# Kernel tuning notes

Hardware: AMD Instinct MI355X
Metric: run time of the kernel (lower is better)

The kernel has to match this reference:

```python
import jax, jax.numpy as jnp
import numpy as np
import math

H, W = 32, 32
HID = 256
K = 4
B = 16
DIN = 272
DFF = 1024
L = 2
NB = 7
IMG_H, IMG_W = 256, 256
LN_EPS = 1e-5


def _layernorm(x, g, b):
    m = jnp.mean(x, axis=-1, keepdims=True)
    v = jnp.var(x, axis=-1, keepdims=True)
    return (x - m) / jnp.sqrt(v + LN_EPS) * g + b


def _neighbor_mask(h, w, nb):
    # (h*w, h*w): 0 inside the nb x nb window around each query pixel, -inf outside
    rr = jnp.repeat(jnp.arange(h), w)
    cc = jnp.tile(jnp.arange(w), h)
    near = (jnp.abs(rr[:, None] - rr[None, :]) <= nb // 2) & (
        jnp.abs(cc[:, None] - cc[None, :]) <= nb // 2
    )
    return jnp.where(near, 0.0, -jnp.inf).astype(jnp.float32)


def _pos_embed(row_embed, col_embed):
    # pos[i*w + j] = concat(col_embed[j], row_embed[i])  -> (h*w, hid)
    h, nf = row_embed.shape
    w = col_embed.shape[0]
    pe = jnp.concatenate(
        [
            jnp.broadcast_to(col_embed[None, :, :], (h, w, nf)),
            jnp.broadcast_to(row_embed[:, None, :], (h, w, nf)),
        ],
        axis=-1,
    )
    return pe.reshape(h * w, 2 * nf)


def _resize_bilinear_ac(x, oh, ow):
    # nn.UpsamplingBilinear2d => align_corners=True
    b, c, h, w = x.shape
    ys = jnp.arange(oh) * ((h - 1) / (oh - 1))
    y0 = jnp.floor(ys).astype(jnp.int32)
    y1 = jnp.minimum(y0 + 1, h - 1)
    fy = (ys - y0).astype(x.dtype)
    x = x[:, :, y0, :] * (1 - fy)[None, None, :, None] + x[:, :, y1, :] * fy[None, None, :, None]
    xs = jnp.arange(ow) * ((w - 1) / (ow - 1))
    x0 = jnp.floor(xs).astype(jnp.int32)
    x1 = jnp.minimum(x0 + 1, w - 1)
    fx = (xs - x0).astype(x.dtype)
    x = x[:, :, :, x0] * (1 - fx) + x[:, :, :, x1] * fx
    return x


def _forward(query_features, matched_features, qW, qb, kvW, kvb, row_embed, col_embed,
             aggW, aggb, n1g, n1b, l1W, l1b, l2W, l2b, n2g, n2b, outW, outb):
    b, c_in, h, w = query_features.shape
    n = h * w
    # b c h w -> b (h w) c, then input projections
    qt = query_features.transpose(0, 2, 3, 1).reshape(b, n, c_in) @ qW + qb  # (b,n,hid)
    kt = matched_features.transpose(0, 1, 3, 4, 2).reshape(K, b, n, c_in) @ kvW + kvb  # (K,b,n,hid)

    pos = _pos_embed(row_embed, col_embed)  # (n, hid); broadcast over batch
    mask = _neighbor_mask(h, w, NB)  # (n, n)
    scale = 1.0 / math.sqrt(qt.shape[-1])

    x = qt
    for l in range(L):
        qp = (x + pos) * scale            # q gets pos embed then scaled
        kp = kt + pos                     # k gets pos embed; v is the raw matched tokens
        scores = jnp.einsum('bnc,kbmc->kbnm', qp, kp) + mask
        attn = jax.nn.softmax(scores, axis=-1)
        o = jnp.einsum('kbnm,kbmc->bnkc', attn, kt).reshape(b, n, K * HID)
        o = o @ aggW[l] + aggb[l]
        x = _layernorm(x + o, n1g[l], n1b[l])
        ff = jax.nn.relu(x @ l1W[l] + l1b[l]) @ l2W[l] + l2b[l]
        x = _layernorm(x + ff, n2g[l], n2b[l])

    recon_tokens = x @ outW + outb  # (b,n,c_in)
    recon = recon_tokens.reshape(b, h, w, c_in).transpose(0, 3, 1, 2)
    pred = jnp.sqrt(jnp.sum((recon - query_features) ** 2, axis=1, keepdims=True))
    pred = (pred - pred.min()) / (pred.max() - pred.min())
    pred = _resize_bilinear_ac(pred, IMG_H, IMG_W)
    return recon, pred


def setup_inputs() -> dict:
    key = jax.random.key(0)
    ks = jax.random.split(key, 12)

    def nrm(k, shape, scale=0.02):
        return jax.random.normal(k, shape, jnp.float32) * scale

    return {
        'query_features': jax.random.normal(ks[0], (B, DIN, H, W), jnp.float32),
        'matched_features': jax.random.normal(ks[1], (K, B, DIN, H, W), jnp.float32),
        'qW': nrm(ks[2], (DIN, HID)), 'qb': jnp.zeros((HID,), jnp.float32),
        'kvW': nrm(ks[3], (DIN, HID)), 'kvb': jnp.zeros((HID,), jnp.float32),
        'row_embed': jax.random.uniform(ks[4], (H, HID // 2), jnp.float32),
        'col_embed': jax.random.uniform(ks[5], (W, HID // 2), jnp.float32),
        'aggW': nrm(ks[6], (L, K * HID, HID)), 'aggb': jnp.zeros((L, HID), jnp.float32),
        'n1g': jnp.ones((L, HID), jnp.float32), 'n1b': jnp.zeros((L, HID), jnp.float32),
        'l1W': nrm(ks[7], (L, HID, DFF)), 'l1b': jnp.zeros((L, DFF), jnp.float32),
        'l2W': nrm(ks[8], (L, DFF, HID)), 'l2b': jnp.zeros((L, HID), jnp.float32),
        'n2g': jnp.ones((L, HID), jnp.float32), 'n2b': jnp.zeros((L, HID), jnp.float32),
        'outW': nrm(ks[9], (HID, DIN)), 'outb': jnp.zeros((DIN,), jnp.float32),
    }


def reference(query_features, matched_features, qW, qb, kvW, kvb, row_embed, col_embed,
              aggW, aggb, n1g, n1b, l1W, l1b, l2W, l2b, n2g, n2b, outW, outb):
    return _forward(query_features, matched_features, qW, qb, kvW, kvb, row_embed,
                    col_embed, aggW, aggb, n1g, n1b, l1W, l1b, l2W, l2b, n2g, n2b,
                    outW, outb)
```

## Files before the change

kernel.cpp:

```cpp
#include <hip/hip_runtime.h>
#include <hip/hip_bf16.h>
#include <math.h>

#define BATCH 16
#define NTOK 1024
#define HID 256
#define KMEM 4
#define DIN 272
#define DINP 288
#define DFF 1024
#define LN_EPS 1e-5f

using short8 = __attribute__((ext_vector_type(8))) short;
using short4v = __attribute__((ext_vector_type(4))) short;
using floatx4 = __attribute__((ext_vector_type(4))) float;

__device__ inline short f2bf(float f) {
  unsigned u = __builtin_bit_cast(unsigned, f);
  u += 0x7fff + ((u >> 16) & 1);
  return (short)(u >> 16);
}
__device__ inline float bf2f(short s) {
  unsigned u = ((unsigned)(unsigned short)s) << 16;
  return __builtin_bit_cast(float, u);
}

#define QSCALE 0.0625f

__global__ __launch_bounds__(256) void pos_kernel(
    const float* __restrict__ row_e, const float* __restrict__ col_e,
    float* __restrict__ pos) {
  int t = blockIdx.x;
  int j = threadIdx.x;
  float v = (j < 128) ? col_e[(t & 31) * 128 + j]
                      : row_e[(t >> 5) * 128 + (j - 128)];
  pos[t * 256 + j] = v;
}

struct WtJob {
  const float* src;
  short* dst;
  int K, Kd, N, ntx, start;
};
struct WtJobs {
  WtJob j[9];
};

__global__ __launch_bounds__(256) void wt_cvt_all_kernel(WtJobs jobs) {
  __shared__ short tile[32][33];
  int bid = blockIdx.x;
  int ji = 0;
#pragma unroll
  for (int i = 1; i < 9; ++i)
    if (bid >= jobs.j[i].start) ji = i;
  const float* W = jobs.j[ji].src;
  short* Wt = jobs.j[ji].dst;
  int K = jobs.j[ji].K, Kd = jobs.j[ji].Kd, N = jobs.j[ji].N;
  int local = bid - jobs.j[ji].start;
  int n0 = (local % jobs.j[ji].ntx) * 32;
  int k0 = (local / jobs.j[ji].ntx) * 32;
  int tx = threadIdx.x & 31, ty8 = threadIdx.x >> 5;
#pragma unroll
  for (int i = 0; i < 4; i++) {
    int k = k0 + ty8 + i * 8;
    int n = n0 + tx;
    float v = (k < K && n < N) ? W[(long)k * N + n] : 0.f;
    tile[ty8 + i * 8][tx] = f2bf(v);
  }
  __syncthreads();
#pragma unroll
  for (int i = 0; i < 4; i++) {
    int n = n0 + ty8 + i * 8;
    int k = k0 + tx;
    if (n < N && k < Kd) Wt[(long)n * Kd + k] = tile[tx][ty8 + i * 8];
  }
}

template <int OUTMODE, bool AFP32>
__global__ __launch_bounds__(256) void gemm2_kernel(
    const void* __restrict__ Ap, const short* __restrict__ Wt,
    const float* __restrict__ bias, float* __restrict__ Cf,
    short* __restrict__ Cs, int M, int N, int K, int gxn,
    short* __restrict__ ktp, short* __restrict__ ktv,
    const float* __restrict__ pos, const float* __restrict__ qfp,
    float* __restrict__ ppart) {
  __shared__ short As[2][64][40];
  __shared__ short Bs[2][128][40];
  __shared__ float part_s[64][2];
  int nwg = gridDim.x;
  int cpx = nwg >> 3;
  int bid = blockIdx.x;
  int h = (bid & 7) * cpx + (bid >> 3);
  int cx = h % gxn;
  int ry = h / gxn;
  int row0 = ry * 64, col0 = cx * 128;
  int tid = threadIdx.x;
  int w = tid >> 6, lane = tid & 63;
  int wrow = (w >> 1) * 32, wcol = (w & 1) * 64;
  int lcol = lane & 15, kg = lane >> 4;

  const short* Ab16 = nullptr;
  const float* Abf = nullptr;
  int arow = tid >> 2, ak = (tid & 3) * 8;
  int atok = tid & 63, acb = (tid >> 6) * 8;
  if (AFP32) {
    int slice = row0 >> 10, tok0 = row0 & 1023;
    Abf = (const float*)Ap + (long)slice * DIN * NTOK + tok0;
  } else {
    Ab16 = (const short*)Ap + (long)row0 * K;
  }
  int brow = tid >> 2, bk = (tid & 3) * 8;
  const short* Bb = Wt + (long)col0 * K;
  bool bv0 = (col0 + brow) < N;
  bool bv1 = (col0 + brow + 64) < N;

  const short8 z8 = (short8){0, 0, 0, 0, 0, 0, 0, 0};
  short8 ra;
  float rf[8];
  short8 rb0, rb1;
  if (AFP32) {
#pragma unroll
    for (int j = 0; j < 8; ++j)
      rf[j] = (acb + j < DIN) ? Abf[(long)(acb + j) * NTOK + atok] : 0.f;
    short8 s;
#pragma unroll
    for (int j = 0; j < 8; ++j) s[j] = f2bf(rf[j]);
    *reinterpret_cast<short8*>(&As[0][atok][acb]) = s;
  } else {
    ra = *reinterpret_cast<const short8*>(&Ab16[(long)arow * K + ak]);
    *reinterpret_cast<short8*>(&As[0][arow][ak]) = ra;
  }
  rb0 = bv0 ? *reinterpret_cast<const short8*>(&Bb[(long)brow * K + bk]) : z8;
  rb1 = bv1 ? *reinterpret_cast<const short8*>(&Bb[(long)(brow + 64) * K + bk])
            : z8;
  *reinterpret_cast<short8*>(&Bs[0][brow][bk]) = rb0;
  *reinterpret_cast<short8*>(&Bs[0][brow + 64][bk]) = rb1;
  __syncthreads();

  floatx4 acc[2][4];
#pragma unroll
  for (int m = 0; m < 2; ++m)
#pragma unroll
    for (int n = 0; n < 4; ++n) acc[m][n] = (floatx4){0.f, 0.f, 0.f, 0.f};

  int NT = K >> 5;
  for (int t = 0; t < NT; ++t) {
    int cur = t & 1;
    if (t + 1 < NT) {
      int ko = (t + 1) << 5;
      if (AFP32) {
#pragma unroll
        for (int j = 0; j < 8; ++j)
          rf[j] = (ko + acb + j < DIN)
                      ? Abf[(long)(ko + acb + j) * NTOK + atok]
                      : 0.f;
      } else {
        ra = *reinterpret_cast<const short8*>(&Ab16[(long)arow * K + ko + ak]);
      }
      rb0 = bv0 ? *reinterpret_cast<const short8*>(&Bb[(long)brow * K + ko + bk])
                : z8;
      rb1 = bv1 ? *reinterpret_cast<const short8*>(
                      &Bb[(long)(brow + 64) * K + ko + bk])
                : z8;
    }
    short8 af[2], bf[4];
#pragma unroll
    for (int m = 0; m < 2; ++m)
      af[m] = *reinterpret_cast<const short8*>(
          &As[cur][wrow + m * 16 + lcol][kg * 8]);
#pragma unroll
    for (int n = 0; n < 4; ++n)
      bf[n] = *reinterpret_cast<const short8*>(
          &Bs[cur][wcol + n * 16 + lcol][kg * 8]);
#pragma unroll
    for (int m = 0; m < 2; ++m)
#pragma unroll
      for (int n = 0; n < 4; ++n)
        acc[m][n] = __builtin_amdgcn_mfma_f32_16x16x32_bf16(af[m], bf[n],
                                                            acc[m][n], 0, 0, 0);
    if (t + 1 < NT) {
      int nxt = cur ^ 1;
      if (AFP32) {
        short8 s;
#pragma unroll
        for (int j = 0; j < 8; ++j) s[j] = f2bf(rf[j]);
        *reinterpret_cast<short8*>(&As[nxt][atok][acb]) = s;
      } else {
        *reinterpret_cast<short8*>(&As[nxt][arow][ak]) = ra;
      }
      *reinterpret_cast<short8*>(&Bs[nxt][brow][bk]) = rb0;
      *reinterpret_cast<short8*>(&Bs[nxt][brow + 64][bk]) = rb1;
    }
    __syncthreads();
  }

  if (OUTMODE == 2) {
    short* Ts = &Bs[0][0][0];
    int slice = row0 >> 10, tok0 = row0 & 1023;
#pragma unroll
    for (int n = 0; n < 4; ++n) {
      int cl = wcol + n * 16 + lcol;
      int c = col0 + cl;
      float bv = bias[c];
#pragma unroll
      for (int m = 0; m < 2; ++m) {
        int rl = wrow + m * 16 + kg * 4;
#pragma unroll
        for (int q = 0; q < 4; ++q) {
          float val = acc[m][n][q] + bv;
          Ts[(rl + q) * 132 + cl] = f2bf(val);
          ktp[(long)(row0 + rl + q) * 256 + c] =
              f2bf(val + pos[(tok0 + rl + q) * 256 + c]);
        }
      }
    }
    __syncthreads();
    int t8 = tid & 7;
#pragma unroll
    for (int p = 0; p < 4; ++p) {
      int cl = p * 32 + (tid >> 3);
      short8 v;
#pragma unroll
      for (int j = 0; j < 8; ++j) v[j] = Ts[(t8 * 8 + j) * 132 + cl];
      *reinterpret_cast<short8*>(
          &ktv[(long)slice * (256 * 1024) + (long)(col0 + cl) * 1024 + tok0 +
               t8 * 8]) = v;
    }
    return;
  }

  if (OUTMODE == 4) {
    int bb = row0 >> 10;
    int tb0 = (row0 & 1023) + wrow;
    float sqp[2][4] = {};
#pragma unroll
    for (int n = 0; n < 4; ++n) {
      int c = col0 + wcol + n * 16 + lcol;
      if (c < N) {
        float bv = bias[c];
#pragma unroll
        for (int m = 0; m < 2; ++m) {
          int tb = tb0 + m * 16 + kg * 4;
          long addr = ((long)bb * DIN + c) * 1024 + tb;
          float4 qv = *reinterpret_cast<const float4*>(&qfp[addr]);
          float4 ov;
          float v0 = acc[m][n][0] + bv;
          float v1 = acc[m][n][1] + bv;
          float v2 = acc[m][n][2] + bv;
          float v3 = acc[m][n][3] + bv;
          ov.x = v0;
          ov.y = v1;
          ov.z = v2;
          ov.w = v3;
          float d0 = v0 - qv.x, d1 = v1 - qv.y, d2 = v2 - qv.z, d3 = v3 - qv.w;
          sqp[m][0] = fmaf(d0, d0, sqp[m][0]);
          sqp[m][1] = fmaf(d1, d1, sqp[m][1]);
          sqp[m][2] = fmaf(d2, d2, sqp[m][2]);
          sqp[m][3] = fmaf(d3, d3, sqp[m][3]);
          *reinterpret_cast<float4*>(&Cf[addr]) = ov;
        }
      }
    }
#pragma unroll
    for (int m = 0; m < 2; ++m)
#pragma unroll
      for (int q = 0; q < 4; ++q) {
        float s = sqp[m][q];
        s += __shfl_xor(s, 1);
        s += __shfl_xor(s, 2);
        s += __shfl_xor(s, 4);
        s += __shfl_xor(s, 8);
        if (lcol == 0) part_s[wrow + m * 16 + kg * 4 + q][w & 1] = s;
      }
    __syncthreads();
    if (tid < 64)
      ppart[(long)cx * 16384 + row0 + tid] = part_s[tid][0] + part_s[tid][1];
    return;
  }

#pragma unroll
  for (int n = 0; n < 4; ++n) {
    int c = col0 + wcol + n * 16 + lcol;
    if (c >= N) continue;
    float bv = bias[c];
#pragma unroll
    for (int m = 0; m < 2; ++m) {
      int rbase = row0 + wrow + m * 16 + kg * 4;
      if (OUTMODE == 0) {
#pragma unroll
        for (int q = 0; q < 4; ++q)
          Cf[(long)(rbase + q) * N + c] = acc[m][n][q] + bv;
      } else if (OUTMODE == 1) {
#pragma unroll
        for (int q = 0; q < 4; ++q)
          Cs[(long)(rbase + q) * N + c] = f2bf(fmaxf(acc[m][n][q] + bv, 0.f));
      } else if (OUTMODE == 3) {
#pragma unroll
        for (int q = 0; q < 4; ++q) {
          float val = acc[m][n][q] + bv;
          Cf[(long)(rbase + q) * N + c] = val;
          Cs[(long)(rbase + q) * N + c] =
              f2bf((val + pos[((rbase + q) & 1023) * 256 + c]) * QSCALE);
        }
      }
    }
  }
}

template <bool EX, bool EQ>
__global__ __launch_bounds__(256) void gemm_ln_kernel(
    const short* __restrict__ A, const short* __restrict__ Wt,
    const float* __restrict__ bias, const float* __restrict__ res,
    const float* __restrict__ g, const float* __restrict__ bta,
    float* __restrict__ xout, short* __restrict__ x16out,
    const float* __restrict__ pos, short* __restrict__ q16out, int K) {
  __shared__ short As[2][32][40];
  __shared__ short Bs[2][256][40];
  __shared__ float st_s[32][4];
  __shared__ float st_s2[32][4];
  int tid = threadIdx.x;
  int row0 = blockIdx.x * 32;
  int w = tid >> 6, lane = tid & 63, lcol = lane & 15, kg = lane >> 4;
  int arow = tid >> 2, ak = (tid & 3) * 8;
  int brow = tid >> 2, bk = (tid & 3) * 8;
  const short* Ab = A + (long)row0 * K;

  short8 ra, rb[4];
  if (tid < 128) ra = *reinterpret_cast<const short8*>(&Ab[(long)arow * K + ak]);
#pragma unroll
  for (int i = 0; i < 4; ++i)
    rb[i] = *reinterpret_cast<const short8*>(&Wt[(long)(brow + i * 64) * K + bk]);
  if (tid < 128) *reinterpret_cast<short8*>(&As[0][arow][ak]) = ra;
#pragma unroll
  for (int i = 0; i < 4; ++i)
    *reinterpret_cast<short8*>(&Bs[0][brow + i * 64][bk]) = rb[i];
  __syncthreads();

  floatx4 acc[2][4];
#pragma unroll
  for (int m = 0; m < 2; ++m)
#pragma unroll
    for (int n = 0; n < 4; ++n) acc[m][n] = (floatx4){0.f, 0.f, 0.f, 0.f};

  int NT = K >> 5;
  for (int t = 0; t < NT; ++t) {
    int cur = t & 1;
    if (t + 1 < NT) {
      int ko = (t + 1) << 5;
      if (tid < 128)
        ra = *reinterpret_cast<const short8*>(&Ab[(long)arow * K + ko + ak]);
#pragma unroll
      for (int i = 0; i < 4; ++i)
        rb[i] = *reinterpret_cast<const short8*>(
            &Wt[(long)(brow + i * 64) * K + ko + bk]);
    }
    short8 af[2], bf[4];
#pragma unroll
    for (int m = 0; m < 2; ++m)
      af[m] =
          *reinterpret_cast<const short8*>(&As[cur][m * 16 + lcol][kg * 8]);
#pragma unroll
    for (int n = 0; n < 4; ++n)
      bf[n] = *reinterpret_cast<const short8*>(
          &Bs[cur][w * 64 + n * 16 + lcol][kg * 8]);
#pragma unroll
    for (int m = 0; m < 2; ++m)
#pragma unroll
      for (int n = 0; n < 4; ++n)
        acc[m][n] = __builtin_amdgcn_mfma_f32_16x16x32_bf16(af[m], bf[n],
                                                            acc[m][n], 0, 0, 0);
    if (t + 1 < NT) {
      int nxt = cur ^ 1;
      if (tid < 128) *reinterpret_cast<short8*>(&As[nxt][arow][ak]) = ra;
#pragma unroll
      for (int i = 0; i < 4; ++i)
        *reinterpret_cast<short8*>(&Bs[nxt][brow + i * 64][bk]) = rb[i];
    }
    __syncthreads();
  }

  float val[2][4][4];
#pragma unroll
  for (int n = 0; n < 4; ++n) {
    int c = w * 64 + n * 16 + lcol;
    float bv = bias[c];
#pragma unroll
    for (int m = 0; m < 2; ++m) {
      int rbase = row0 + m * 16 + kg * 4;
#pragma unroll
      for (int q = 0; q < 4; ++q)
        val[m][n][q] = acc[m][n][q] + bv + res[(long)(rbase + q) * 256 + c];
    }
  }
  float s[2][4], s2[2][4];
#pragma unroll
  for (int m = 0; m < 2; ++m)
#pragma unroll
    for (int q = 0; q < 4; ++q) {
      float ss = 0.f, ss2 = 0.f;
#pragma unroll
      for (int n = 0; n < 4; ++n) {
        float v = val[m][n][q];
        ss += v;
        ss2 = fmaf(v, v, ss2);
      }
      ss += __shfl_xor(ss, 1);
      ss2 += __shfl_xor(ss2, 1);
      ss += __shfl_xor(ss, 2);
      ss2 += __shfl_xor(ss2, 2);
      ss += __shfl_xor(ss, 4);
      ss2 += __shfl_xor(ss2, 4);
      ss += __shfl_xor(ss, 8);
      ss2 += __shfl_xor(ss2, 8);
      s[m][q] = ss;
      s2[m][q] = ss2;
    }
  if (lcol == 0) {
#pragma unroll
    for (int m = 0; m < 2; ++m)
#pragma unroll
      for (int q = 0; q < 4; ++q) {
        st_s[m * 16 + kg * 4 + q][w] = s[m][q];
        st_s2[m * 16 + kg * 4 + q][w] = s2[m][q];
      }
  }
  __syncthreads();
#pragma unroll
  for (int m = 0; m < 2; ++m)
#pragma unroll
    for (int q = 0; q < 4; ++q) {
      int row = m * 16 + kg * 4 + q;
      float4 a4 = *reinterpret_cast<const float4*>(&st_s[row][0]);
      float4 b4 = *reinterpret_cast<const float4*>(&st_s2[row][0]);
      float S = (a4.x + a4.y) + (a4.z + a4.w);
      float S2 = (b4.x + b4.y) + (b4.z + b4.w);
      float mean = S * (1.f / 256.f);
      float var = S2 * (1.f / 256.f) - mean * mean;
      float inv = rsqrtf(var + LN_EPS);
#pragma unroll
      for (int n = 0; n < 4; ++n) {
        int c = w * 64 + n * 16 + lcol;
        float o = (val[m][n][q] - mean) * inv * g[c] + bta[c];
        long addr = (long)(row0 + row) * 256 + c;
        if (EX) xout[addr] = o;
        x16out[addr] = f2bf(o);
        if (EQ)
          q16out[addr] =
              f2bf((o + pos[((row0 + row) & 1023) * 256 + c]) * QSCALE);
      }
    }
}

__global__ __launch_bounds__(256) void attn_kernel(
    const short* __restrict__ q16, const short* __restrict__ ktp,
    const short* __restrict__ ktv, short* __restrict__ o) {
  __shared__ short QP_s[32][264];
  __shared__ float st_mx[32][4];
  __shared__ float st_sm[32][4];
  int h = blockIdx.x;
  int xcd = h & 7, jj = h >> 3;
  int sidx = xcd * 8 + (jj >> 5);
  int r = jj & 31;
  int b = sidx & 15, k = sidx >> 4;
  int tid = threadIdx.x;
  int w = tid >> 6, lane = tid & 63, lcol = lane & 15, kg = lane >> 4;

  int r0 = max(r - 3, 0), r1 = min(r + 3, 31);
  int nkr = r1 - r0 + 1, nm = nkr * 32;
  const short* qb = q16 + ((long)b * NTOK + r * 32) * HID;
  const short* ktpb = ktp + ((long)(k * BATCH + b)) * NTOK * HID;
  const short* ktvb = ktv + ((long)(k * BATCH + b)) * NTOK * HID;

#pragma unroll
  for (int p = 0; p < 4; ++p) {
    int chunk = p * 256 + tid;
    int row = chunk >> 5, c8 = (chunk & 31) * 8;
    short8 v = *reinterpret_cast<const short8*>(&qb[(long)row * HID + c8]);
    *reinterpret_cast<short8*>(&QP_s[row][c8]) = v;
  }
  __syncthreads();

  floatx4 acc[2][4];
#pragma unroll
  for (int m = 0; m < 2; ++m)
#pragma unroll
    for (int n = 0; n < 4; ++n) acc[m][n] = (floatx4){0.f, 0.f, 0.f, 0.f};

  int tokn[4];
#pragma unroll
  for (int n = 0; n < 4; ++n) {
    int nf = w * 4 + n;
    int krow = min(r0 + (nf >> 1), 31);
    tokn[n] = krow * 32 + ((nf & 1) << 4) + lcol;
  }
#pragma unroll
  for (int s = 0; s < 8; ++s) {
    short8 af0 = *reinterpret_cast<const short8*>(&QP_s[lcol][s * 32 + kg * 8]);
    short8 af1 =
        *reinterpret_cast<const short8*>(&QP_s[16 + lcol][s * 32 + kg * 8]);
#pragma unroll
    for (int n = 0; n < 4; ++n) {
      short8 bfr = *reinterpret_cast<const short8*>(
          &ktpb[(long)tokn[n] * HID + s * 32 + kg * 8]);
      acc[0][n] =
          __builtin_amdgcn_mfma_f32_16x16x32_bf16(af0, bfr, acc[0][n], 0, 0, 0);
      acc[1][n] =
          __builtin_amdgcn_mfma_f32_16x16x32_bf16(af1, bfr, acc[1][n], 0, 0, 0);
    }
  }

  const float NEG = -3.0e38f;
  float mx[2][4];
#pragma unroll
  for (int m = 0; m < 2; ++m)
#pragma unroll
    for (int q = 0; q < 4; ++q) {
      int rr = m * 16 + kg * 4 + q;
      float vmax = NEG;
#pragma unroll
      for (int n = 0; n < 4; ++n) {
        int col = (w * 4 + n) * 16 + lcol;
        int ck = col & 31;
        bool ok = (col < nm) && (ck - rr <= 3) && (rr - ck <= 3);
        float v = ok ? acc[m][n][q] : NEG;
        acc[m][n][q] = v;
        vmax = fmaxf(vmax, v);
      }
      vmax = fmaxf(vmax, __shfl_xor(vmax, 1));
      vmax = fmaxf(vmax, __shfl_xor(vmax, 2));
      vmax = fmaxf(vmax, __shfl_xor(vmax, 4));
      vmax = fmaxf(vmax, __shfl_xor(vmax, 8));
      mx[m][q] = vmax;
    }
  if (lcol == 0) {
#pragma unroll
    for (int m = 0; m < 2; ++m)
#pragma unroll
      for (int q = 0; q < 4; ++q) st_mx[m * 16 + kg * 4 + q][w] = mx[m][q];
  }
  __syncthreads();
  float sm[2][4];
#pragma unroll
  for (int m = 0; m < 2; ++m)
#pragma unroll
    for (int q = 0; q < 4; ++q) {
      int rr = m * 16 + kg * 4 + q;
      float4 v4 = *reinterpret_cast<const float4*>(&st_mx[rr][0]);
      float g = fmaxf(fmaxf(v4.x, v4.y), fmaxf(v4.z, v4.w));
      float ss = 0.f;
#pragma unroll
      for (int n = 0; n < 4; ++n) {
        float v = acc[m][n][q];
        float pv = (v > -1.0e30f) ? exp2f((v - g) * 1.4426950408889634f) : 0.f;
        acc[m][n][q] = pv;
        ss += pv;
      }
      ss += __shfl_xor(ss, 1);
      ss += __shfl_xor(ss, 2);
      ss += __shfl_xor(ss, 4);
      ss += __shfl_xor(ss, 8);
      sm[m][q] = ss;
    }
  if (lcol == 0) {
#pragma unroll
    for (int m = 0; m < 2; ++m)
#pragma unroll
      for (int q = 0; q < 4; ++q) st_sm[m * 16 + kg * 4 + q][w] = sm[m][q];
  }
  __syncthreads();
#pragma unroll
  for (int m = 0; m < 2; ++m)
#pragma unroll
    for (int q = 0; q < 4; ++q) {
      int rr = m * 16 + kg * 4 + q;
      float4 v4 = *reinterpret_cast<const float4*>(&st_sm[rr][0]);
      float rinv = 1.0f / (v4.x + v4.y + v4.z + v4.w);
#pragma unroll
      for (int n = 0; n < 4; ++n) {
        QP_s[rr][(w * 4 + n) * 16 + lcol] = f2bf(acc[m][n][q] * rinv);
      }
    }
  __syncthreads();

  floatx4 oacc[2][4];
#pragma unroll
  for (int m = 0; m < 2; ++m)
#pragma unroll
    for (int n = 0; n < 4; ++n) oacc[m][n] = (floatx4){0.f, 0.f, 0.f, 0.f};

  for (int kb = 0; kb < nkr; ++kb) {
    short8 ap0 = *reinterpret_cast<const short8*>(&QP_s[lcol][kb * 32 + kg * 8]);
    short8 ap1 =
        *reinterpret_cast<const short8*>(&QP_s[16 + lcol][kb * 32 + kg * 8]);
    int tokb = (r0 + kb) * 32;
#pragma unroll
    for (int n = 0; n < 4; ++n) {
      int ch = w * 64 + n * 16 + lcol;
      short8 bv = *reinterpret_cast<const short8*>(
          &ktvb[(long)ch * NTOK + tokb + kg * 8]);
      oacc[0][n] =
          __builtin_amdgcn_mfma_f32_16x16x32_bf16(ap0, bv, oacc[0][n], 0, 0, 0);
      oacc[1][n] =
          __builtin_amdgcn_mfma_f32_16x16x32_bf16(ap1, bv, oacc[1][n], 0, 0, 0);
    }
  }
#pragma unroll
  for (int m = 0; m < 2; ++m)
#pragma unroll
    for (int n = 0; n < 4; ++n) {
      int ch = w * 64 + n * 16 + lcol;
#pragma unroll
      for (int q = 0; q < 4; ++q) {
        int rr = m * 16 + kg * 4 + q;
        o[((long)b * NTOK + r * 32 + rr) * (KMEM * HID) + k * HID + ch] =
            f2bf(oacc[m][n][q]);
      }
    }
}

__global__ __launch_bounds__(256) void minmax_kernel(
    const float* __restrict__ ppart, float* __restrict__ pred_sq,
    float* __restrict__ mnmx) {
  int tid = threadIdx.x;
  float mn = INFINITY, mx = -INFINITY;
  for (int i = tid; i < BATCH * NTOK; i += 256) {
    float v = ppart[i] + ppart[16384 + i] + ppart[32768 + i];
    pred_sq[i] = v;
    float sv = sqrtf(v);
    mn = fminf(mn, sv);
    mx = fmaxf(mx, sv);
  }
#pragma unroll
  for (int off = 32; off > 0; off >>= 1) {
    mn = fminf(mn, __shfl_xor(mn, off));
    mx = fmaxf(mx, __shfl_xor(mx, off));
  }
  __shared__ float smn[4], smx[4];
  int wave = tid >> 6, lane = tid & 63;
  if (lane == 0) {
    smn[wave] = mn;
    smx[wave] = mx;
  }
  __syncthreads();
  if (tid == 0) {
    mn = fminf(fminf(smn[0], smn[1]), fminf(smn[2], smn[3]));
    mx = fmaxf(fmaxf(smx[0], smx[1]), fmaxf(smx[2], smx[3]));
    mnmx[0] = mn;
    mnmx[1] = mx;
  }
}

__global__ __launch_bounds__(256) void resize_kernel(
    const float* __restrict__ pred_sq, const float* __restrict__ mnmx,
    float* __restrict__ out) {
  long idx = (long)blockIdx.x * 256 + threadIdx.x;
  if (idx >= (long)BATCH * 256 * 256) return;
  int b = (int)(idx >> 16);
  int oy = (int)((idx >> 8) & 255), ox = (int)(idx & 255);
  float mn = mnmx[0], mx = mnmx[1];
  float inv = 1.0f / (mx - mn);
  float ys = oy * (31.0f / 255.0f);
  int y0 = (int)floorf(ys);
  int y1 = min(y0 + 1, 31);
  float fy = ys - (float)y0;
  float xs = ox * (31.0f / 255.0f);
  int x0 = (int)floorf(xs);
  int x1 = min(x0 + 1, 31);
  float fx = xs - (float)x0;
  const float* p = pred_sq + b * NTOK;
  float v00 = sqrtf(p[y0 * 32 + x0]), v01 = sqrtf(p[y0 * 32 + x1]);
  float v10 = sqrtf(p[y1 * 32 + x0]), v11 = sqrtf(p[y1 * 32 + x1]);
  float cA = v00 * (1.f - fy) + v10 * fy;
  float cB = v01 * (1.f - fy) + v11 * fy;
  float v = cA * (1.f - fx) + cB * fx;
  out[idx] = (v - mn) * inv;
}

extern "C" void kernel_launch(void* const* d_in, const int* in_sizes, int n_in,
                              void* d_out, int out_size, void* d_ws,
                              size_t ws_size, hipStream_t stream) {
  const float* qf = (const float*)d_in[0];
  const float* mf = (const float*)d_in[1];
  const float* qW = (const float*)d_in[2];
  const float* qb = (const float*)d_in[3];
  const float* kvW = (const float*)d_in[4];
  const float* kvb = (const float*)d_in[5];
  const float* row_e = (const float*)d_in[6];
  const float* col_e = (const float*)d_in[7];
  const float* aggW = (const float*)d_in[8];
  const float* aggb = (const float*)d_in[9];
  const float* n1g = (const float*)d_in[10];
  const float* n1b = (const float*)d_in[11];
  const float* l1W = (const float*)d_in[12];
  const float* l1b = (const float*)d_in[13];
  const float* l2W = (const float*)d_in[14];
  const float* l2b = (const float*)d_in[15];
  const float* n2g = (const float*)d_in[16];
  const float* n2b = (const float*)d_in[17];
  const float* outW = (const float*)d_in[18];
  const float* outb = (const float*)d_in[19];

  float* out = (float*)d_out;
  float* recon = out;
  float* pred = out + (long)BATCH * DIN * NTOK;

  float* ws = (float*)d_ws;
  float* pos = ws;
  float* x = pos + 262144;
  short* x16 = (short*)(x + 4194304);
  short* q16 = x16 + 4194304;
  short* ktp = q16 + 4194304;
  short* ktv = ktp + 16777216;
  short* buf16 = ktv + 16777216;
  float* tmp256 = (float*)(buf16 + 16777216);
  short* wt = (short*)(tmp256 + 4194304);
  short* wt_agg0 = wt;
  short* wt_agg1 = wt_agg0 + 262144;
  short* wt_l1_0 = wt_agg1 + 262144;
  short* wt_l1_1 = wt_l1_0 + 262144;
  short* wt_l2_0 = wt_l1_1 + 262144;
  short* wt_l2_1 = wt_l2_0 + 262144;
  short* wt_out = wt_l2_1 + 262144;
  short* wt_q = wt_out + 69632;
  short* wt_kv = wt_q + 73728;
  float* pred_part = (float*)(wt_kv + 73728);
  float* pred_sq = pred_part + 49152;
  float* mnmx = pred_sq + 16384;

  pos_kernel<<<NTOK, 256, 0, stream>>>(row_e, col_e, pos);

  {
    WtJobs jobs;
    jobs.j[0] = {aggW, wt_agg0, 1024, 1024, 256, 8, 0};
    jobs.j[1] = {aggW + 262144, wt_agg1, 1024, 1024, 256, 8, 256};
    jobs.j[2] = {l1W, wt_l1_0, 256, 256, 1024, 32, 512};
    jobs.j[3] = {l1W + 262144, wt_l1_1, 256, 256, 1024, 32, 768};
    jobs.j[4] = {l2W, wt_l2_0, 1024, 1024, 256, 8, 1024};
    jobs.j[5] = {l2W + 262144, wt_l2_1, 1024, 1024, 256, 8, 1280};
    jobs.j[6] = {outW, wt_out, 256, 256, 272, 9, 1536};
    jobs.j[7] = {qW, wt_q, 272, 288, 256, 8, 1608};
    jobs.j[8] = {kvW, wt_kv, 272, 288, 256, 8, 1680};
    wt_cvt_all_kernel<<<1752, 256, 0, stream>>>(jobs);
  }

  gemm2_kernel<3, true><<<512, 256, 0, stream>>>(
      qf, wt_q, qb, x, q16, BATCH * NTOK, HID, DINP, 2, nullptr, nullptr, pos,
      nullptr, nullptr);
  gemm2_kernel<2, true><<<2048, 256, 0, stream>>>(
      mf, wt_kv, kvb, nullptr, nullptr, KMEM * BATCH * NTOK, HID, DINP, 2, ktp,
      ktv, pos, nullptr, nullptr);

  for (int l = 0; l < 2; l++) {
    attn_kernel<<<2048, 256, 0, stream>>>(q16, ktp, ktv, buf16);
    gemm_ln_kernel<true, false><<<512, 256, 0, stream>>>(
        buf16, l ? wt_agg1 : wt_agg0, aggb + l * 256, x, n1g + l * 256,
        n1b + l * 256, x, x16, nullptr, nullptr, KMEM * HID);
    gemm2_kernel<1, false><<<2048, 256, 0, stream>>>(
        x16, l ? wt_l1_1 : wt_l1_0, l1b + l * 1024, nullptr, buf16,
        BATCH * NTOK, DFF, HID, 8, nullptr, nullptr, nullptr, nullptr,
        nullptr);
    if (l == 0) {
      gemm_ln_kernel<true, true><<<512, 256, 0, stream>>>(
          buf16, wt_l2_0, l2b, x, n2g, n2b, x, x16, pos, q16, DFF);
    } else {
      gemm_ln_kernel<false, false><<<512, 256, 0, stream>>>(
          buf16, wt_l2_1, l2b + 256, x, n2g + 256, n2b + 256, x, x16, nullptr,
          nullptr, DFF);
    }
  }

  gemm2_kernel<4, false><<<768, 256, 0, stream>>>(
      x16, wt_out, outb, recon, nullptr, BATCH * NTOK, DIN, HID, 3, nullptr,
      nullptr, nullptr, qf, pred_part);
  minmax_kernel<<<1, 256, 0, stream>>>(pred_part, pred_sq, mnmx);
  resize_kernel<<<(BATCH * 256 * 256) / 256, 256, 0, stream>>>(pred_sq, mnmx,
                                                               pred);
}
```

Measured before the change: 396.5 us.

## Use a full-width K/V projection kernel and keep the residual stream in bf16

Replaces the generic two-column-tile K/V projection with a dedicated kernel whose 64x256 tile covers all 256 output columns. Each block now reads its fp32 matched-feature rows once instead of once per column tile. Separately, the fp32 residual buffer `x` is removed: the q projection and the LayerNorm GEMMs read and write the residual only as bf16 (`x16`), in place. This cuts global read/write traffic per layer, at the cost of accumulating the residual in bf16 precision.

```diff
diff --git a/kernel.cpp b/kernel.cpp
--- a/kernel.cpp
+++ b/kernel.cpp
@@ -76,14 +76,130 @@
   }
 }
 
+__global__ __launch_bounds__(256) void kvproj_kernel(
+    const float* __restrict__ mf, const short* __restrict__ Wt,
+    const float* __restrict__ bias, short* __restrict__ ktp,
+    short* __restrict__ ktv, const float* __restrict__ pos) {
+  __shared__ short As[2][64][40];
+  __shared__ short Bs[2][256][40];
+  int nwg = gridDim.x;
+  int bid = blockIdx.x;
+  int h = (bid & 7) * (nwg >> 3) + (bid >> 3);
+  int row0 = h * 64;
+  int slice = row0 >> 10, tok0 = row0 & 1023;
+  int tid = threadIdx.x;
+  int w = tid >> 6, lane = tid & 63;
+  int lcol = lane & 15, kg = lane >> 4;
+  int wcol = w * 64;
+
+  const float* Abf = mf + (long)slice * DIN * NTOK + tok0;
+  int atok = tid & 63, acb = (tid >> 6) * 8;
+  int brow = tid >> 2, bk = (tid & 3) * 8;
+
+  float rf[8];
+  short8 rb[4];
+#pragma unroll
+  for (int j = 0; j < 8; ++j)
+    rf[j] = (acb + j < DIN) ? Abf[(long)(acb + j) * NTOK + atok] : 0.f;
+  {
+    short8 s;
+#pragma unroll
+    for (int j = 0; j < 8; ++j) s[j] = f2bf(rf[j]);
+    *reinterpret_cast<short8*>(&As[0][atok][acb]) = s;
+  }
+#pragma unroll
+  for (int i = 0; i < 4; ++i) {
+    rb[i] = *reinterpret_cast<const short8*>(
+        &Wt[(long)(brow + i * 64) * DINP + bk]);
+    *reinterpret_cast<short8*>(&Bs[0][brow + i * 64][bk]) = rb[i];
+  }
+  __syncthreads();
+
+  floatx4 acc[4][4];
+#pragma unroll
+  for (int m = 0; m < 4; ++m)
+#pragma unroll
+    for (int n = 0; n < 4; ++n) acc[m][n] = (floatx4){0.f, 0.f, 0.f, 0.f};
+
+  const int NT = DINP >> 5;
+  for (int t = 0; t < NT; ++t) {
+    int cur = t & 1;
+    if (t + 1 < NT) {
+      int ko = (t + 1) << 5;
+#pragma unroll
+      for (int j = 0; j < 8; ++j)
+        rf[j] = (ko + acb + j < DIN) ? Abf[(long)(ko + acb + j) * NTOK + atok]
+                                     : 0.f;
+#pragma unroll
+      for (int i = 0; i < 4; ++i)
+        rb[i] = *reinterpret_cast<const short8*>(
+            &Wt[(long)(brow + i * 64) * DINP + ko + bk]);
+    }
+    short8 af[4], bf[4];
+#pragma unroll
+    for (int m = 0; m < 4; ++m)
+      af[m] = *reinterpret_cast<const short8*>(
+          &As[cur][m * 16 + lcol][kg * 8]);
+#pragma unroll
+    for (int n = 0; n < 4; ++n)
+      bf[n] = *reinterpret_cast<const short8*>(
+          &Bs[cur][wcol + n * 16 + lcol][kg * 8]);
+#pragma unroll
+    for (int m = 0; m < 4; ++m)
+#pragma unroll
+      for (int n = 0; n < 4; ++n)
+        acc[m][n] = __builtin_amdgcn_mfma_f32_16x16x32_bf16(af[m], bf[n],
+                                                            acc[m][n], 0, 0, 0);
+    if (t + 1 < NT) {
+      int nxt = cur ^ 1;
+      short8 s;
+#pragma unroll
+      for (int j = 0; j < 8; ++j) s[j] = f2bf(rf[j]);
+      *reinterpret_cast<short8*>(&As[nxt][atok][acb]) = s;
+#pragma unroll
+      for (int i = 0; i < 4; ++i)
+        *reinterpret_cast<short8*>(&Bs[nxt][brow + i * 64][bk]) = rb[i];
+    }
+    __syncthreads();
+  }
+
+  short* Ts = &Bs[0][0][0];
+#pragma unroll
+  for (int n = 0; n < 4; ++n) {
+    int cl = wcol + n * 16 + lcol;
+    float bv = bias[cl];
+#pragma unroll
+    for (int m = 0; m < 4; ++m) {
+      int rl = m * 16 + kg * 4;
+#pragma unroll
+      for (int q = 0; q < 4; ++q) {
+        float val = acc[m][n][q] + bv;
+        Ts[(rl + q) * 260 + cl] = f2bf(val);
+        ktp[(long)(row0 + rl + q) * 256 + cl] =
+            f2bf(val + pos[(tok0 + rl + q) * 256 + cl]);
+      }
+    }
+  }
+  __syncthreads();
+  int t8 = tid & 7;
+#pragma unroll
+  for (int p = 0; p < 8; ++p) {
+    int cl = p * 32 + (tid >> 3);
+    short8 v;
+#pragma unroll
+    for (int j = 0; j < 8; ++j) v[j] = Ts[(t8 * 8 + j) * 260 + cl];
+    *reinterpret_cast<short8*>(&ktv[(long)slice * (256 * 1024) +
+                                    (long)cl * 1024 + tok0 + t8 * 8]) = v;
+  }
+}
+
 template <int OUTMODE, bool AFP32>
 __global__ __launch_bounds__(256) void gemm2_kernel(
     const void* __restrict__ Ap, const short* __restrict__ Wt,
     const float* __restrict__ bias, float* __restrict__ Cf,
     short* __restrict__ Cs, int M, int N, int K, int gxn,
-    short* __restrict__ ktp, short* __restrict__ ktv,
-    const float* __restrict__ pos, const float* __restrict__ qfp,
-    float* __restrict__ ppart) {
+    short* __restrict__ q16p, const float* __restrict__ pos,
+    const float* __restrict__ qfp, float* __restrict__ ppart) {
   __shared__ short As[2][64][40];
   __shared__ short Bs[2][128][40];
   __shared__ float part_s[64][2];
@@ -192,41 +308,6 @@
       *reinterpret_cast<short8*>(&Bs[nxt][brow + 64][bk]) = rb1;
     }
     __syncthreads();
-  }
-
-  if (OUTMODE == 2) {
-    short* Ts = &Bs[0][0][0];
-    int slice = row0 >> 10, tok0 = row0 & 1023;
-#pragma unroll
-    for (int n = 0; n < 4; ++n) {
-      int cl = wcol + n * 16 + lcol;
-      int c = col0 + cl;
-      float bv = bias[c];
-#pragma unroll
-      for (int m = 0; m < 2; ++m) {
-        int rl = wrow + m * 16 + kg * 4;
-#pragma unroll
-        for (int q = 0; q < 4; ++q) {
-          float val = acc[m][n][q] + bv;
-          Ts[(rl + q) * 132 + cl] = f2bf(val);
-          ktp[(long)(row0 + rl + q) * 256 + c] =
-              f2bf(val + pos[(tok0 + rl + q) * 256 + c]);
-        }
-      }
-    }
-    __syncthreads();
-    int t8 = tid & 7;
-#pragma unroll
-    for (int p = 0; p < 4; ++p) {
-      int cl = p * 32 + (tid >> 3);
-      short8 v;
-#pragma unroll
-      for (int j = 0; j < 8; ++j) v[j] = Ts[(t8 * 8 + j) * 132 + cl];
-      *reinterpret_cast<short8*>(
-          &ktv[(long)slice * (256 * 1024) + (long)(col0 + cl) * 1024 + tok0 +
-               t8 * 8]) = v;
-    }
-    return;
   }
 
   if (OUTMODE == 4) {
@@ -286,11 +367,7 @@
 #pragma unroll
     for (int m = 0; m < 2; ++m) {
       int rbase = row0 + wrow + m * 16 + kg * 4;
-      if (OUTMODE == 0) {
-#pragma unroll
-        for (int q = 0; q < 4; ++q)
-          Cf[(long)(rbase + q) * N + c] = acc[m][n][q] + bv;
-      } else if (OUTMODE == 1) {
+      if (OUTMODE == 1) {
 #pragma unroll
         for (int q = 0; q < 4; ++q)
           Cs[(long)(rbase + q) * N + c] = f2bf(fmaxf(acc[m][n][q] + bv, 0.f));
@@ -298,8 +375,8 @@
 #pragma unroll
         for (int q = 0; q < 4; ++q) {
           float val = acc[m][n][q] + bv;
-          Cf[(long)(rbase + q) * N + c] = val;
-          Cs[(long)(rbase + q) * N + c] =
+          Cs[(long)(rbase + q) * N + c] = f2bf(val);
+          q16p[(long)(rbase + q) * N + c] =
               f2bf((val + pos[((rbase + q) & 1023) * 256 + c]) * QSCALE);
         }
       }
@@ -307,13 +384,13 @@
   }
 }
 
-template <bool EX, bool EQ>
+template <bool EQ>
 __global__ __launch_bounds__(256) void gemm_ln_kernel(
     const short* __restrict__ A, const short* __restrict__ Wt,
-    const float* __restrict__ bias, const float* __restrict__ res,
+    const float* __restrict__ bias, const short* __restrict__ res16,
     const float* __restrict__ g, const float* __restrict__ bta,
-    float* __restrict__ xout, short* __restrict__ x16out,
-    const float* __restrict__ pos, short* __restrict__ q16out, int K) {
+    short* __restrict__ x16out, const float* __restrict__ pos,
+    short* __restrict__ q16out, int K) {
   __shared__ short As[2][32][40];
   __shared__ short Bs[2][256][40];
   __shared__ float st_s[32][4];
@@ -389,7 +466,8 @@
       int rbase = row0 + m * 16 + kg * 4;
 #pragma unroll
       for (int q = 0; q < 4; ++q)
-        val[m][n][q] = acc[m][n][q] + bv + res[(long)(rbase + q) * 256 + c];
+        val[m][n][q] =
+            acc[m][n][q] + bv + bf2f(res16[(long)(rbase + q) * 256 + c]);
     }
   }
   float s[2][4], s2[2][4];
@@ -442,7 +520,6 @@
         int c = w * 64 + n * 16 + lcol;
         float o = (val[m][n][q] - mean) * inv * g[c] + bta[c];
         long addr = (long)(row0 + row) * 256 + c;
-        if (EX) xout[addr] = o;
         x16out[addr] = f2bf(o);
         if (EQ)
           q16out[addr] =
@@ -706,14 +783,12 @@
 
   float* ws = (float*)d_ws;
   float* pos = ws;
-  float* x = pos + 262144;
-  short* x16 = (short*)(x + 4194304);
+  short* x16 = (short*)(pos + 262144);
   short* q16 = x16 + 4194304;
   short* ktp = q16 + 4194304;
   short* ktv = ktp + 16777216;
   short* buf16 = ktv + 16777216;
-  float* tmp256 = (float*)(buf16 + 16777216);
-  short* wt = (short*)(tmp256 + 4194304);
+  short* wt = buf16 + 16777216;
   short* wt_agg0 = wt;
   short* wt_agg1 = wt_agg0 + 262144;
   short* wt_l1_0 = wt_agg1 + 262144;
@@ -744,34 +819,31 @@
   }
 
   gemm2_kernel<3, true><<<512, 256, 0, stream>>>(
-      qf, wt_q, qb, x, q16, BATCH * NTOK, HID, DINP, 2, nullptr, nullptr, pos,
+      qf, wt_q, qb, nullptr, x16, BATCH * NTOK, HID, DINP, 2, q16, pos,
       nullptr, nullptr);
-  gemm2_kernel<2, true><<<2048, 256, 0, stream>>>(
-      mf, wt_kv, kvb, nullptr, nullptr, KMEM * BATCH * NTOK, HID, DINP, 2, ktp,
-      ktv, pos, nullptr, nullptr);
+  kvproj_kernel<<<1024, 256, 0, stream>>>(mf, wt_kv, kvb, ktp, ktv, pos);
 
   for (int l = 0; l < 2; l++) {
     attn_kernel<<<2048, 256, 0, stream>>>(q16, ktp, ktv, buf16);
-    gemm_ln_kernel<true, false><<<512, 256, 0, stream>>>(
-        buf16, l ? wt_agg1 : wt_agg0, aggb + l * 256, x, n1g + l * 256,
-        n1b + l * 256, x, x16, nullptr, nullptr, KMEM * HID);
+    gemm_ln_kernel<false><<<512, 256, 0, stream>>>(
+        buf16, l ? wt_agg1 : wt_agg0, aggb + l * 256, x16, n1g + l * 256,
+        n1b + l * 256, x16, nullptr, nullptr, KMEM * HID);
     gemm2_kernel<1, false><<<2048, 256, 0, stream>>>(
         x16, l ? wt_l1_1 : wt_l1_0, l1b + l * 1024, nullptr, buf16,
-        BATCH * NTOK, DFF, HID, 8, nullptr, nullptr, nullptr, nullptr,
-        nullptr);
+        BATCH * NTOK, DFF, HID, 8, nullptr, nullptr, nullptr, nullptr);
     if (l == 0) {
-      gemm_ln_kernel<true, true><<<512, 256, 0, stream>>>(
-          buf16, wt_l2_0, l2b, x, n2g, n2b, x, x16, pos, q16, DFF);
+      gemm_ln_kernel<true><<<512, 256, 0, stream>>>(
+          buf16, wt_l2_0, l2b, x16, n2g, n2b, x16, pos, q16, DFF);
     } else {
-      gemm_ln_kernel<false, false><<<512, 256, 0, stream>>>(
-          buf16, wt_l2_1, l2b + 256, x, n2g + 256, n2b + 256, x, x16, nullptr,
+      gemm_ln_kernel<false><<<512, 256, 0, stream>>>(
+          buf16, wt_l2_1, l2b + 256, x16, n2g + 256, n2b + 256, x16, nullptr,
           nullptr, DFF);
     }
   }
 
   gemm2_kernel<4, false><<<768, 256, 0, stream>>>(
       x16, wt_out, outb, recon, nullptr, BATCH * NTOK, DIN, HID, 3, nullptr,
-      nullptr, nullptr, qf, pred_part);
+      nullptr, qf, pred_part);
   minmax_kernel<<<1, 256, 0, stream>>>(pred_part, pred_sq, mnmx);
   resize_kernel<<<(BATCH * 256 * 256) / 256, 256, 0, stream>>>(pred_sq, mnmx,
                                                                pred);
```

After: 402.5 us. No clear change (+1.5%).
